# Performance work log

Hardware: AMD Instinct MI355X
Metric: run time of the kernel (lower is better)

Reference implementation:

```python
import jax, jax.numpy as jnp
import numpy as np

# Irreps layout: x = [32x0e | 16x1o] -> dim 32 + 48 = 80; sh = [1x0e | 1x1o] -> dim 4
MUL0, MUL1 = 32, 16
DIM = MUL0 + 3 * MUL1            # 80
E, N = 100000, 10000             # edges, nodes
EDGE_DIM, HIDDEN = 32, 64
# e3nn instruction order (i_in1 outer, i_in2 inner):
#   A: 0e x 0e -> 0e  (MUL0*MUL0)
#   C: 0e x 1o -> 1o  (MUL0*MUL1)
#   D: 1o x 0e -> 1o  (MUL1*MUL1)
#   B: 1o x 1o -> 0e  (MUL1*MUL0)
NA = MUL0 * MUL0
NC = MUL0 * MUL1
ND = MUL1 * MUL1
NB = MUL1 * MUL0
WNUM = NA + NC + ND + NB         # tp.weight_numel = 2304
INV_SQRT3 = 1.0 / np.sqrt(3.0).astype(np.float32)   # CG (1,1,0) = delta/sqrt(3)
NORM = np.float32(1.0 / np.sqrt(MUL0 + MUL1))        # element path norm: fan-in = 32+16 = 48 for both outputs


def setup_inputs() -> dict:
    key = jax.random.key(0)
    ks = jax.random.split(key, 10)
    return {
        "dst": jax.random.randint(ks[0], (E,), 0, N),
        "x_src": jax.random.normal(ks[1], (E, DIM), jnp.float32),
        "x_dst": jax.random.normal(ks[2], (N, DIM), jnp.float32),
        "sh": jax.random.normal(ks[3], (E, 4), jnp.float32),
        "edge_attr": jax.random.normal(ks[4], (E, EDGE_DIM), jnp.float32),
        "mlp_w1": jax.random.normal(ks[5], (EDGE_DIM, HIDDEN), jnp.float32) / np.sqrt(EDGE_DIM),
        "mlp_b1": jnp.zeros((HIDDEN,), jnp.float32),
        "mlp_w2": jax.random.normal(ks[6], (HIDDEN, WNUM), jnp.float32) / np.sqrt(HIDDEN),
        "mlp_b2": jnp.zeros((WNUM,), jnp.float32),
        "res_w0": jax.random.normal(ks[7], (MUL0, MUL0), jnp.float32),
        "res_w1": jax.random.normal(ks[8], (MUL1, MUL1), jnp.float32),
    }


def reference(dst, x_src, x_dst, sh, edge_attr, mlp_w1, mlp_b1, mlp_w2, mlp_b2, res_w0, res_w1):
    e = x_src.shape[0]
    n = x_dst.shape[0]
    # edge MLP -> per-edge tensor-product weights
    h = jax.nn.relu(edge_attr @ mlp_w1 + mlp_b1)
    w = h @ mlp_w2 + mlp_b2                              # [E, WNUM]
    wa = w[:, :NA].reshape(e, MUL0, MUL0)                # 0e x 0e -> 0e
    wc = w[:, NA:NA + NC].reshape(e, MUL0, MUL1)         # 0e x 1o -> 1o
    wd = w[:, NA + NC:NA + NC + ND].reshape(e, MUL1, MUL1)  # 1o x 0e -> 1o
    wb = w[:, NA + NC + ND:].reshape(e, MUL1, MUL0)      # 1o x 1o -> 0e

    x0 = x_src[:, :MUL0]                                 # [E, 32]
    x1 = x_src[:, MUL0:].reshape(e, MUL1, 3)             # [E, 16, 3]
    sh0 = sh[:, 0]                                       # [E]
    sh1 = sh[:, 1:4]                                     # [E, 3]

    # equivariant tensor product with per-edge weights
    out0 = NORM * (jnp.einsum('euw,eu,e->ew', wa, x0, sh0)
                   + INV_SQRT3 * jnp.einsum('euw,eum,em->ew', wb, x1, sh1))   # [E, 32]
    out1 = NORM * (jnp.einsum('euw,eu,em->ewm', wc, x0, sh1)
                   + jnp.einsum('euw,eum,e->ewm', wd, x1, sh0))               # [E, 16, 3]
    msg = jnp.concatenate([out0, out1.reshape(e, 3 * MUL1)], axis=-1)        # [E, 80]

    # scatter-mean to destination nodes
    sums = jax.ops.segment_sum(msg, dst, num_segments=n)                      # [N, 80]
    cnt = jax.ops.segment_sum(jnp.ones((e,), msg.dtype), dst, num_segments=n)
    mean = sums / jnp.maximum(cnt, 1.0)[:, None]

    # residual: e3nn Linear (per-irrep, fan-in normalized)
    r0 = (x_dst[:, :MUL0] @ res_w0) / np.sqrt(MUL0)
    r1 = jnp.einsum('num,uw->nwm', x_dst[:, MUL0:].reshape(n, MUL1, 3), res_w1) / np.sqrt(MUL1)
    res = jnp.concatenate([r0, r1.reshape(n, 3 * MUL1)], axis=-1)

    return res + mean
```

## Files before the change

kernel.cpp:

```cpp
#include <hip/hip_runtime.h>
#include <hip/hip_bf16.h>

#define E_TOT   100000
#define N_NODES 10000
#define DIMV    80
#define HID     64
#define EDIM    32
#define WNUM    2304
#define TE      32

static constexpr float NORMF      = 0.14433756729740643f;
static constexpr float INV_SQRT3F = 0.57735026918962576f;
static constexpr float RS32       = 0.17677669529663687f;
static constexpr float RS16       = 0.25f;

typedef __attribute__((ext_vector_type(8))) short bf16x8;
typedef __attribute__((ext_vector_type(4))) float f32x4;

static __device__ __forceinline__ ushort f2bf(float v) {
    __hip_bfloat16 h(v);
    return *reinterpret_cast<ushort*>(&h);
}

__global__ __launch_bounds__(256) void prep_w2t(const float* __restrict__ W2,
                                                ushort* __restrict__ W2T) {
    __shared__ float sT[64][65];
    const int j0 = blockIdx.x * 64;
    #pragma unroll
    for (int k = 0; k < 16; ++k) {
        int idx = threadIdx.x + k*256;
        int t = idx >> 6, j = idx & 63;
        sT[j][t] = W2[t*WNUM + j0 + j];
    }
    __syncthreads();
    #pragma unroll
    for (int k = 0; k < 16; ++k) {
        int idx = threadIdx.x + k*256;
        int j = idx >> 6, t = idx & 63;
        W2T[(size_t)(j0 + j)*64 + t] = f2bf(sT[j][t]);
    }
}

__global__ __launch_bounds__(256) void edge_kernel(
    const int* __restrict__ dst, const float* __restrict__ x_src,
    const float* __restrict__ sh, const float* __restrict__ ea,
    const float* __restrict__ W1, const float* __restrict__ b1,
    const ushort* __restrict__ W2T, const float* __restrict__ b2,
    float* __restrict__ sums, float* __restrict__ cnt)
{
    __shared__ float  sX[TE][81];
    __shared__ float  sSh[TE][4];
    __shared__ float  sXs1[TE][17];
    __shared__ float  sEcA[TE][33];
    __shared__ ushort sHbf[TE][HID];
    __shared__ float  sMsg[TE][84];
    __shared__ int    sDst[TE];

    const int tid  = threadIdx.x;
    const int lane = tid & 63;
    const int wave = tid >> 6;
    const int e0   = blockIdx.x * TE;

    for (int i = tid; i < TE*DIMV; i += 256) { int e = i/80, k = i-e*80; sX[e][k] = x_src[e0*DIMV + i]; }
    for (int i = tid; i < TE*EDIM; i += 256) { int e = i>>5, k = i&31; sEcA[e][k] = ea[e0*EDIM + i]; }
    for (int i = tid; i < TE*4;    i += 256) sSh[0][i] = sh[e0*4 + i];
    if (tid < TE) sDst[tid] = dst[e0 + tid];
    __syncthreads();

    #pragma unroll
    for (int k = 0; k < (TE*HID)/256; ++k) {
        int idx = tid + k*256;
        int e = idx >> 6, t = idx & 63;
        float h = b1[t];
        #pragma unroll
        for (int i = 0; i < EDIM; ++i) h = fmaf(sEcA[e][i], W1[i*HID + t], h);
        sHbf[e][t] = f2bf(fmaxf(h, 0.f));
    }
    __syncthreads();

    for (int i = tid; i < TE*32; i += 256) {
        int e = i >> 5, u = i & 31;
        sEcA[e][u] = sSh[e][0] * sX[e][u];
    }
    for (int i = tid; i < TE*16; i += 256) {
        int e = i >> 4, u = i & 15;
        sXs1[e][u] = INV_SQRT3F * (sX[e][32+u*3+0]*sSh[e][1] +
                                   sX[e][32+u*3+1]*sSh[e][2] +
                                   sX[e][32+u*3+2]*sSh[e][3]);
    }
    for (int i = tid; i < TE*84; i += 256) sMsg[0][i] = 0.f;
    __syncthreads();

    const int c     = lane & 15;
    const int g     = lane >> 4;
    const int rbase = g << 2;
    bf16x8 afrag[2][2];
    #pragma unroll
    for (int rt = 0; rt < 2; ++rt)
        #pragma unroll
        for (int kt = 0; kt < 2; ++kt)
            afrag[rt][kt] = *reinterpret_cast<const bf16x8*>(&sHbf[rt*16 + c][kt*32 + g*8]);

    float pA[8]     = {};
    float sC2[8]    = {};
    float sDv[8][3] = {};

    bf16x8 nb0, nb1;
    float  nbv;
    {
        const int t16 = wave;
        const ushort* bp = W2T + (((size_t)((t16 << 4) + c)) << 6) + (g << 3);
        nb0 = *reinterpret_cast<const bf16x8*>(bp);
        nb1 = *reinterpret_cast<const bf16x8*>(bp + 32);
        nbv = b2[(t16 << 4) + c];
    }
    #pragma unroll
    for (int k = 0; k < 36; ++k) {
        const bf16x8 cb0 = nb0;
        const bf16x8 cb1 = nb1;
        const float  cbv = nbv;
        if (k < 35) {
            const int t16n = wave + ((k + 1) << 2);
            const ushort* bp = W2T + (((size_t)((t16n << 4) + c)) << 6) + (g << 3);
            nb0 = *reinterpret_cast<const bf16x8*>(bp);
            nb1 = *reinterpret_cast<const bf16x8*>(bp + 32);
            nbv = b2[(t16n << 4) + c];
        }
        f32x4 a0 = {cbv, cbv, cbv, cbv};
        f32x4 a1 = {cbv, cbv, cbv, cbv};
        a0 = __builtin_amdgcn_mfma_f32_16x16x32_bf16(afrag[0][0], cb0, a0, 0, 0, 0);
        a0 = __builtin_amdgcn_mfma_f32_16x16x32_bf16(afrag[0][1], cb1, a0, 0, 0, 0);
        a1 = __builtin_amdgcn_mfma_f32_16x16x32_bf16(afrag[1][0], cb0, a1, 0, 0, 0);
        a1 = __builtin_amdgcn_mfma_f32_16x16x32_bf16(afrag[1][1], cb1, a1, 0, 0, 0);

        const int t16 = wave + (k << 2);
        if (k < 16) {
            const int u = t16 >> 1;
            #pragma unroll
            for (int r = 0; r < 4; ++r) {
                pA[r]   = fmaf(sEcA[rbase + r][u],      a0[r], pA[r]);
                pA[4+r] = fmaf(sEcA[16 + rbase + r][u], a1[r], pA[4+r]);
            }
        } else if (k < 24) {
            const int u = t16 - 64;
            #pragma unroll
            for (int r = 0; r < 4; ++r) {
                sC2[r]   = fmaf(sX[rbase + r][u],      a0[r], sC2[r]);
                sC2[4+r] = fmaf(sX[16 + rbase + r][u], a1[r], sC2[4+r]);
            }
        } else if (k < 28) {
            const int u = t16 - 96;
            #pragma unroll
            for (int r = 0; r < 4; ++r) {
                #pragma unroll
                for (int m = 0; m < 3; ++m) {
                    sDv[r][m]   = fmaf(sX[rbase + r][32 + u*3 + m],      a0[r], sDv[r][m]);
                    sDv[4+r][m] = fmaf(sX[16 + rbase + r][32 + u*3 + m], a1[r], sDv[4+r][m]);
                }
            }
        } else {
            const int u = (t16 - 112) >> 1;
            #pragma unroll
            for (int r = 0; r < 4; ++r) {
                pA[r]   = fmaf(sXs1[rbase + r][u],      a0[r], pA[r]);
                pA[4+r] = fmaf(sXs1[16 + rbase + r][u], a1[r], pA[4+r]);
            }
        }
    }

    const int wcol = c + ((wave & 1) << 4);
    #pragma unroll
    for (int rt = 0; rt < 2; ++rt) {
        #pragma unroll
        for (int r = 0; r < 4; ++r) {
            const int e = rt*16 + rbase + r;
            const int s = rt*4 + r;
            atomicAdd(&sMsg[e][wcol], pA[s]);
            const float s0 = sSh[e][0];
            atomicAdd(&sMsg[e][32 + c*3 + 0], sSh[e][1]*sC2[s] + s0*sDv[s][0]);
            atomicAdd(&sMsg[e][32 + c*3 + 1], sSh[e][2]*sC2[s] + s0*sDv[s][1]);
            atomicAdd(&sMsg[e][32 + c*3 + 2], sSh[e][3]*sC2[s] + s0*sDv[s][2]);
        }
    }
    __syncthreads();

    for (int i = tid; i < TE*DIMV; i += 256) {
        int e = i / DIMV, k = i - e*DIMV;
        atomicAdd(&sums[sDst[e]*DIMV + k], NORMF * sMsg[e][k]);
    }
    if (tid < TE) atomicAdd(&cnt[sDst[tid]], 1.0f);
}

__global__ __launch_bounds__(256) void node_kernel(
    const float* __restrict__ x_dst, const float* __restrict__ rw0,
    const float* __restrict__ rw1, const float* __restrict__ sums,
    const float* __restrict__ cnt, float* __restrict__ out)
{
    int gid = blockIdx.x*256 + threadIdx.x;
    if (gid >= N_NODES*DIMV) return;
    int n = gid / DIMV;
    int k = gid - n*DIMV;
    const float* xd = x_dst + n*DIMV;
    float r = 0.f;
    if (k < 32) {
        #pragma unroll
        for (int u = 0; u < 32; ++u) r = fmaf(xd[u], rw0[u*32 + k], r);
        r *= RS32;
    } else {
        int kk = k - 32;
        int w = kk / 3, m = kk - w*3;
        #pragma unroll
        for (int u = 0; u < 16; ++u) r = fmaf(xd[32 + u*3 + m], rw1[u*16 + w], r);
        r *= RS16;
    }
    float cc = cnt[n];
    out[gid] = r + sums[gid] / fmaxf(cc, 1.f);
}

extern "C" void kernel_launch(void* const* d_in, const int* in_sizes, int n_in,
                              void* d_out, int out_size, void* d_ws, size_t ws_size,
                              hipStream_t stream) {
    const int*   dst   = (const int*)  d_in[0];
    const float* x_src = (const float*)d_in[1];
    const float* x_dst = (const float*)d_in[2];
    const float* sh    = (const float*)d_in[3];
    const float* ea    = (const float*)d_in[4];
    const float* W1    = (const float*)d_in[5];
    const float* b1    = (const float*)d_in[6];
    const float* W2    = (const float*)d_in[7];
    const float* b2    = (const float*)d_in[8];
    const float* rw0   = (const float*)d_in[9];
    const float* rw1   = (const float*)d_in[10];
    float* out  = (float*)d_out;
    char*  ws   = (char*)d_ws;

    float*  sums = (float*)ws;
    float*  cnt  = sums + (size_t)N_NODES*DIMV;
    ushort* W2T  = (ushort*)(ws + (size_t)(N_NODES*DIMV + N_NODES)*sizeof(float));

    hipMemsetAsync(ws, 0, (size_t)(N_NODES*DIMV + N_NODES)*sizeof(float), stream);
    prep_w2t<<<WNUM/64, 256, 0, stream>>>(W2, W2T);
    edge_kernel<<<E_TOT/TE, 256, 0, stream>>>(dst, x_src, sh, ea, W1, b1, W2T, b2, sums, cnt);
    node_kernel<<<(N_NODES*DIMV + 255)/256, 256, 0, stream>>>(x_dst, rw0, rw1, sums, cnt, out);
}
```

Baseline: 383.4 us.

## Double edge tile to 64, compute edge MLP layer 1 with MFMA, share LDS pool

```diff
diff --git a/kernel.cpp b/kernel.cpp
--- a/kernel.cpp
+++ b/kernel.cpp
@@ -7,7 +7,8 @@
 #define HID     64
 #define EDIM    32
 #define WNUM    2304
-#define TE      32
+#define TE      64
+#define NBLK    ((E_TOT + TE - 1) / TE)
 
 static constexpr float NORMF      = 0.14433756729740643f;
 static constexpr float INV_SQRT3F = 0.57735026918962576f;
@@ -41,80 +42,100 @@
     }
 }
 
+__global__ __launch_bounds__(256) void prep_w1t(const float* __restrict__ W1,
+                                                ushort* __restrict__ W1T) {
+    int idx = blockIdx.x*256 + threadIdx.x;
+    if (idx < HID*EDIM) {
+        int t = idx >> 5, i = idx & 31;
+        W1T[idx] = f2bf(W1[i*HID + t]);
+    }
+}
+
 __global__ __launch_bounds__(256) void edge_kernel(
     const int* __restrict__ dst, const float* __restrict__ x_src,
     const float* __restrict__ sh, const float* __restrict__ ea,
-    const float* __restrict__ W1, const float* __restrict__ b1,
+    const float* __restrict__ b1, const ushort* __restrict__ W1T,
     const ushort* __restrict__ W2T, const float* __restrict__ b2,
     float* __restrict__ sums, float* __restrict__ cnt)
 {
-    __shared__ float  sX[TE][81];
+    __shared__ float  sPool[TE][84];
     __shared__ float  sSh[TE][4];
     __shared__ float  sXs1[TE][17];
     __shared__ float  sEcA[TE][33];
-    __shared__ ushort sHbf[TE][HID];
-    __shared__ float  sMsg[TE][84];
+    __shared__ ushort sHbf[TE][72];
+    __shared__ ushort sEAb[TE][40];
     __shared__ int    sDst[TE];
 
     const int tid  = threadIdx.x;
     const int lane = tid & 63;
     const int wave = tid >> 6;
     const int e0   = blockIdx.x * TE;
-
-    for (int i = tid; i < TE*DIMV; i += 256) { int e = i/80, k = i-e*80; sX[e][k] = x_src[e0*DIMV + i]; }
-    for (int i = tid; i < TE*EDIM; i += 256) { int e = i>>5, k = i&31; sEcA[e][k] = ea[e0*EDIM + i]; }
-    for (int i = tid; i < TE*4;    i += 256) sSh[0][i] = sh[e0*4 + i];
-    if (tid < TE) sDst[tid] = dst[e0 + tid];
-    __syncthreads();
-
-    #pragma unroll
-    for (int k = 0; k < (TE*HID)/256; ++k) {
-        int idx = tid + k*256;
-        int e = idx >> 6, t = idx & 63;
-        float h = b1[t];
-        #pragma unroll
-        for (int i = 0; i < EDIM; ++i) h = fmaf(sEcA[e][i], W1[i*HID + t], h);
-        sHbf[e][t] = f2bf(fmaxf(h, 0.f));
+    const int c    = lane & 15;
+    const int g    = lane >> 4;
+    const int rbase = g << 2;
+
+    for (int i = tid; i < TE*DIMV; i += 256) {
+        int e = i/80, k = i - e*80, ge = e0 + e;
+        sPool[e][k] = (ge < E_TOT) ? x_src[(size_t)ge*DIMV + k] : 0.f;
+    }
+    for (int i = tid; i < TE*EDIM; i += 256) {
+        int e = i >> 5, k = i & 31, ge = e0 + e;
+        sEAb[e][k] = (ge < E_TOT) ? f2bf(ea[(size_t)ge*EDIM + k]) : (ushort)0;
+    }
+    for (int i = tid; i < TE*4; i += 256) {
+        int e = i >> 2, k = i & 3, ge = e0 + e;
+        sSh[e][k] = (ge < E_TOT) ? sh[(size_t)ge*4 + k] : 0.f;
+    }
+    if (tid < TE) sDst[tid] = (e0 + tid < E_TOT) ? dst[e0 + tid] : -1;
+    __syncthreads();
+
+    {
+        const float bv1 = b1[wave*16 + c];
+        const f32x4 hinit = {bv1, bv1, bv1, bv1};
+        const bf16x8 bw1 = *reinterpret_cast<const bf16x8*>(&W1T[(wave*16 + c)*EDIM + g*8]);
+        #pragma unroll
+        for (int eb = 0; eb < 4; ++eb) {
+            bf16x8 aea = *reinterpret_cast<const bf16x8*>(&sEAb[eb*16 + c][g*8]);
+            f32x4 h = __builtin_amdgcn_mfma_f32_16x16x32_bf16(aea, bw1, hinit, 0, 0, 0);
+            #pragma unroll
+            for (int r = 0; r < 4; ++r)
+                sHbf[eb*16 + g*4 + r][wave*16 + c] = f2bf(fmaxf(h[r], 0.f));
+        }
     }
     __syncthreads();
 
     for (int i = tid; i < TE*32; i += 256) {
         int e = i >> 5, u = i & 31;
-        sEcA[e][u] = sSh[e][0] * sX[e][u];
+        sEcA[e][u] = sSh[e][0] * sPool[e][u];
     }
     for (int i = tid; i < TE*16; i += 256) {
         int e = i >> 4, u = i & 15;
-        sXs1[e][u] = INV_SQRT3F * (sX[e][32+u*3+0]*sSh[e][1] +
-                                   sX[e][32+u*3+1]*sSh[e][2] +
-                                   sX[e][32+u*3+2]*sSh[e][3]);
-    }
-    for (int i = tid; i < TE*84; i += 256) sMsg[0][i] = 0.f;
-    __syncthreads();
-
-    const int c     = lane & 15;
-    const int g     = lane >> 4;
-    const int rbase = g << 2;
-    bf16x8 afrag[2][2];
-    #pragma unroll
-    for (int rt = 0; rt < 2; ++rt)
+        sXs1[e][u] = INV_SQRT3F * (sPool[e][32+u*3+0]*sSh[e][1] +
+                                   sPool[e][32+u*3+1]*sSh[e][2] +
+                                   sPool[e][32+u*3+2]*sSh[e][3]);
+    }
+    __syncthreads();
+
+    bf16x8 af[4][2];
+    #pragma unroll
+    for (int rt = 0; rt < 4; ++rt)
         #pragma unroll
         for (int kt = 0; kt < 2; ++kt)
-            afrag[rt][kt] = *reinterpret_cast<const bf16x8*>(&sHbf[rt*16 + c][kt*32 + g*8]);
-
-    float pA[8]     = {};
-    float sC2[8]    = {};
-    float sDv[8][3] = {};
+            af[rt][kt] = *reinterpret_cast<const bf16x8*>(&sHbf[rt*16 + c][kt*32 + g*8]);
+
+    float pA[16]     = {};
+    float sC2[16]    = {};
+    float sDv[16][3] = {};
 
     bf16x8 nb0, nb1;
     float  nbv;
     {
-        const int t16 = wave;
-        const ushort* bp = W2T + (((size_t)((t16 << 4) + c)) << 6) + (g << 3);
+        const ushort* bp = W2T + (((size_t)((wave << 4) + c)) << 6) + (g << 3);
         nb0 = *reinterpret_cast<const bf16x8*>(bp);
         nb1 = *reinterpret_cast<const bf16x8*>(bp + 32);
-        nbv = b2[(t16 << 4) + c];
-    }
-    #pragma unroll
+        nbv = b2[(wave << 4) + c];
+    }
+    #pragma unroll 4
     for (int k = 0; k < 36; ++k) {
         const bf16x8 cb0 = nb0;
         const bf16x8 cb1 = nb1;
@@ -126,69 +147,74 @@
             nb1 = *reinterpret_cast<const bf16x8*>(bp + 32);
             nbv = b2[(t16n << 4) + c];
         }
-        f32x4 a0 = {cbv, cbv, cbv, cbv};
-        f32x4 a1 = {cbv, cbv, cbv, cbv};
-        a0 = __builtin_amdgcn_mfma_f32_16x16x32_bf16(afrag[0][0], cb0, a0, 0, 0, 0);
-        a0 = __builtin_amdgcn_mfma_f32_16x16x32_bf16(afrag[0][1], cb1, a0, 0, 0, 0);
-        a1 = __builtin_amdgcn_mfma_f32_16x16x32_bf16(afrag[1][0], cb0, a1, 0, 0, 0);
-        a1 = __builtin_amdgcn_mfma_f32_16x16x32_bf16(afrag[1][1], cb1, a1, 0, 0, 0);
-
+        f32x4 acc[4];
+        #pragma unroll
+        for (int rt = 0; rt < 4; ++rt) {
+            acc[rt] = {cbv, cbv, cbv, cbv};
+            acc[rt] = __builtin_amdgcn_mfma_f32_16x16x32_bf16(af[rt][0], cb0, acc[rt], 0, 0, 0);
+            acc[rt] = __builtin_amdgcn_mfma_f32_16x16x32_bf16(af[rt][1], cb1, acc[rt], 0, 0, 0);
+        }
         const int t16 = wave + (k << 2);
         if (k < 16) {
             const int u = t16 >> 1;
             #pragma unroll
-            for (int r = 0; r < 4; ++r) {
-                pA[r]   = fmaf(sEcA[rbase + r][u],      a0[r], pA[r]);
-                pA[4+r] = fmaf(sEcA[16 + rbase + r][u], a1[r], pA[4+r]);
-            }
+            for (int rt = 0; rt < 4; ++rt)
+                #pragma unroll
+                for (int r = 0; r < 4; ++r)
+                    pA[rt*4+r] = fmaf(sEcA[rt*16 + rbase + r][u], acc[rt][r], pA[rt*4+r]);
         } else if (k < 24) {
             const int u = t16 - 64;
             #pragma unroll
-            for (int r = 0; r < 4; ++r) {
-                sC2[r]   = fmaf(sX[rbase + r][u],      a0[r], sC2[r]);
-                sC2[4+r] = fmaf(sX[16 + rbase + r][u], a1[r], sC2[4+r]);
-            }
+            for (int rt = 0; rt < 4; ++rt)
+                #pragma unroll
+                for (int r = 0; r < 4; ++r)
+                    sC2[rt*4+r] = fmaf(sPool[rt*16 + rbase + r][u], acc[rt][r], sC2[rt*4+r]);
         } else if (k < 28) {
             const int u = t16 - 96;
             #pragma unroll
-            for (int r = 0; r < 4; ++r) {
-                #pragma unroll
-                for (int m = 0; m < 3; ++m) {
-                    sDv[r][m]   = fmaf(sX[rbase + r][32 + u*3 + m],      a0[r], sDv[r][m]);
-                    sDv[4+r][m] = fmaf(sX[16 + rbase + r][32 + u*3 + m], a1[r], sDv[4+r][m]);
+            for (int rt = 0; rt < 4; ++rt)
+                #pragma unroll
+                for (int r = 0; r < 4; ++r) {
+                    const int e = rt*16 + rbase + r, s = rt*4 + r;
+                    #pragma unroll
+                    for (int m = 0; m < 3; ++m)
+                        sDv[s][m] = fmaf(sPool[e][32 + u*3 + m], acc[rt][r], sDv[s][m]);
                 }
-            }
         } else {
             const int u = (t16 - 112) >> 1;
             #pragma unroll
-            for (int r = 0; r < 4; ++r) {
-                pA[r]   = fmaf(sXs1[rbase + r][u],      a0[r], pA[r]);
-                pA[4+r] = fmaf(sXs1[16 + rbase + r][u], a1[r], pA[4+r]);
-            }
-        }
-    }
+            for (int rt = 0; rt < 4; ++rt)
+                #pragma unroll
+                for (int r = 0; r < 4; ++r)
+                    pA[rt*4+r] = fmaf(sXs1[rt*16 + rbase + r][u], acc[rt][r], pA[rt*4+r]);
+        }
+    }
+
+    __syncthreads();
+    for (int i = tid; i < TE*84; i += 256) (&sPool[0][0])[i] = 0.f;
+    __syncthreads();
 
     const int wcol = c + ((wave & 1) << 4);
     #pragma unroll
-    for (int rt = 0; rt < 2; ++rt) {
+    for (int rt = 0; rt < 4; ++rt) {
         #pragma unroll
         for (int r = 0; r < 4; ++r) {
             const int e = rt*16 + rbase + r;
             const int s = rt*4 + r;
-            atomicAdd(&sMsg[e][wcol], pA[s]);
+            atomicAdd(&sPool[e][wcol], pA[s]);
             const float s0 = sSh[e][0];
-            atomicAdd(&sMsg[e][32 + c*3 + 0], sSh[e][1]*sC2[s] + s0*sDv[s][0]);
-            atomicAdd(&sMsg[e][32 + c*3 + 1], sSh[e][2]*sC2[s] + s0*sDv[s][1]);
-            atomicAdd(&sMsg[e][32 + c*3 + 2], sSh[e][3]*sC2[s] + s0*sDv[s][2]);
+            atomicAdd(&sPool[e][32 + c*3 + 0], sSh[e][1]*sC2[s] + s0*sDv[s][0]);
+            atomicAdd(&sPool[e][32 + c*3 + 1], sSh[e][2]*sC2[s] + s0*sDv[s][1]);
+            atomicAdd(&sPool[e][32 + c*3 + 2], sSh[e][3]*sC2[s] + s0*sDv[s][2]);
         }
     }
     __syncthreads();
 
     for (int i = tid; i < TE*DIMV; i += 256) {
         int e = i / DIMV, k = i - e*DIMV;
-        atomicAdd(&sums[sDst[e]*DIMV + k], NORMF * sMsg[e][k]);
-    }
-    if (tid < TE) atomicAdd(&cnt[sDst[tid]], 1.0f);
+        if (sDst[e] >= 0) atomicAdd(&sums[sDst[e]*DIMV + k], NORMF * sPool[e][k]);
+    }
+    if (tid < TE && sDst[tid] >= 0) atomicAdd(&cnt[sDst[tid]], 1.0f);
 }
 
 __global__ __launch_bounds__(256) void node_kernel(
@@ -237,9 +263,11 @@
     float*  sums = (float*)ws;
     float*  cnt  = sums + (size_t)N_NODES*DIMV;
     ushort* W2T  = (ushort*)(ws + (size_t)(N_NODES*DIMV + N_NODES)*sizeof(float));
+    ushort* W1T  = W2T + (size_t)WNUM*HID;
 
     hipMemsetAsync(ws, 0, (size_t)(N_NODES*DIMV + N_NODES)*sizeof(float), stream);
     prep_w2t<<<WNUM/64, 256, 0, stream>>>(W2, W2T);
-    edge_kernel<<<E_TOT/TE, 256, 0, stream>>>(dst, x_src, sh, ea, W1, b1, W2T, b2, sums, cnt);
+    prep_w1t<<<(HID*EDIM + 255)/256, 256, 0, stream>>>(W1, W1T);
+    edge_kernel<<<NBLK, 256, 0, stream>>>(dst, x_src, sh, ea, b1, W1T, W2T, b2, sums, cnt);
     node_kernel<<<(N_NODES*DIMV + 255)/256, 256, 0, stream>>>(x_dst, rw0, rw1, sums, cnt, out);
 }
```

Result: slower. 440.3 us (+14.8%).
